# Performance work log

Hardware: AMD Instinct MI355X
Metric: run time of the kernel (lower is better)

The kernel has to match this reference:

```python
import jax, jax.numpy as jnp
import numpy as np

B, T, Rn, D, O, E, H, C, TM = 20, 20, 20, 4096, 16, 512, 8, 68, 1900


def l2norm(x, axis=-1, eps=1e-12):
    return x / jnp.maximum(jnp.linalg.norm(x, axis=axis, keepdims=True), eps)


def setup_inputs() -> dict:
    key = jax.random.key(0)
    ks = jax.random.split(key, 10)
    return {
        "features": jax.random.normal(ks[0], (B, T, Rn, D), jnp.float32),
        "labels": jax.random.randint(ks[1], (B, O), 0, C),
        "temporal_mem": jax.random.normal(ks[2], (TM, T, D), jnp.float32),
        "entity_W": jax.random.normal(ks[3], (C, E), jnp.float32) / np.float32(np.sqrt(C)),
        "entity_b": jnp.zeros((E,), jnp.float32),
        "Wq": jax.random.normal(ks[4], (E, E), jnp.float32) / np.float32(np.sqrt(E)),
        "Wk": jax.random.normal(ks[5], (D, E), jnp.float32) / np.float32(np.sqrt(D)),
        "Wv": jax.random.normal(ks[6], (D, E), jnp.float32) / np.float32(np.sqrt(D)),
        "Wo": jax.random.normal(ks[7], (E, E), jnp.float32) / np.float32(np.sqrt(E)),
        "obj_W1": jax.random.normal(ks[8], (D, E), jnp.float32) / np.float32(np.sqrt(D)),
        "obj_b1": jnp.zeros((E,), jnp.float32),
        "obj_W2": jax.random.normal(ks[9], (E, 1), jnp.float32) / np.float32(np.sqrt(E)),
        "obj_b2": jnp.zeros((1,), jnp.float32),
    }


def reference(features, labels, temporal_mem, entity_W, entity_b, Wq, Wk, Wv, Wo,
              obj_W1, obj_b1, obj_W2, obj_b2):
    beta = 0.5   # loss mixing weight (module's beta)
    qgce = 0.7   # generalized-CE exponent
    Dh = E // H
    # region features, L2-normalized (dataset_feat == 'CVPR' path)
    Rf = l2norm(features)                                   # [B,T,Rn,D]

    # ---- temporal memory-bank kNN retrieval ----
    R_max = l2norm(jnp.max(Rf, axis=2))                     # [B,T,D] max-pool over regions
    mem_max = l2norm(jnp.max(temporal_mem, axis=1))         # [TM,D] max-pool over frames
    sim = jnp.einsum('btd,md->btm', R_max, mem_max)         # [B,T,TM]
    idx = jnp.argmax(sim, axis=-1)                          # [B,T] nearest memory slot
    Rp = temporal_mem[idx]                                  # [B,T,T,D] gathered memory videos
    mem_feat = jnp.max(Rp, axis=2)                          # [B,T,D]

    # ---- entity (object-label) embedding: one-hot with class 0 zeroed ----
    onehot = jax.nn.one_hot(labels, C, dtype=features.dtype)
    onehot = onehot * (labels != 0)[..., None].astype(features.dtype)
    Qe = onehot @ entity_W + entity_b                       # [B,O,E]

    # ---- multi-head attention fusion over regions + retrieved memory ----
    kv = jnp.concatenate([Rf.reshape(B, T * Rn, D), mem_feat], axis=1)  # [B,N,D]
    q = (Qe @ Wq).reshape(B, O, H, Dh)
    k = (kv @ Wk).reshape(B, -1, H, Dh)
    v = (kv @ Wv).reshape(B, -1, H, Dh)
    scores = jnp.einsum('bohd,bnhd->bhon', q, k) / np.float32(np.sqrt(Dh))
    attn = jax.nn.softmax(scores, axis=-1)
    fused = jnp.einsum('bhon,bnhd->bohd', attn, v).reshape(B, O, E) @ Wo  # [B,O,E]

    # ---- top-k region objectness selection + generalized CE ----
    QR = jax.lax.stop_gradient(jnp.mean(scores, axis=1)[:, :, :T * Rn].reshape(B, O, T, Rn))
    hi = jnp.argmax(QR, axis=-1)                            # [B,O,T] top-1 region
    lo = jnp.argmin(QR, axis=-1)                            # [B,O,T] low region
    bidx = jnp.arange(B)[:, None, None]
    tidx = jnp.arange(T)[None, None, :]
    R_high = Rf[bidx, tidx, hi]                             # [B,O,T,D]
    R_low = Rf[bidx, tidx, lo]                              # [B,O,T,D]
    osel = (labels != 0).astype(features.dtype)             # [B,O]
    onum = jnp.maximum(jnp.sum(osel, axis=1), 1.0)
    mlp = lambda x: jax.nn.sigmoid(jnp.tanh(x @ obj_W1 + obj_b1) @ obj_W2 + obj_b2)
    s_hi = mlp(R_high * osel[..., None, None]).squeeze(-1)  # [B,O,T]
    s_lo = mlp(R_low * osel[..., None, None]).squeeze(-1)
    gce_hi = jnp.mean((1.0 - (s_hi + 1e-7) ** qgce) / qgce * osel[..., None], axis=-1)
    gce_lo = jnp.mean((1.0 - (1.0 - s_lo + 1e-7) ** qgce) / qgce * osel[..., None], axis=-1)
    gce = jnp.mean(jnp.sum(gce_hi, axis=1) / onum) + jnp.mean(jnp.sum(gce_lo, axis=1) / onum)

    return fused + beta * gce
```

## Files before the change

kernel.cpp:

```cpp
#include <hip/hip_runtime.h>

#define B_   20
#define T_   20
#define RN   20
#define D_   4096
#define O_   16
#define E_   512
#define H_   8
#define DH   64
#define TM_  1900
#define NKV  420
#define MROWS (B_*NKV)
#define MPAD 8448
#define NW   1536
#define NSIM 1920
#define MSIM 512
#define CAP  256
#define SIMK 8

using f32x4  = __attribute__((ext_vector_type(4))) float;
using bf16x8 = __attribute__((ext_vector_type(8))) __bf16;

__device__ __forceinline__ unsigned short f2bf(float f){
  unsigned u = __float_as_uint(f);
  u += 0x7fffu + ((u >> 16) & 1u);
  return (unsigned short)(u >> 16);
}

__device__ __forceinline__ void st_bf4(unsigned short* dst, float4 v){
  ushort4 o = make_ushort4(f2bf(v.x), f2bf(v.y), f2bf(v.z), f2bf(v.w));
  *(ushort4*)dst = o;
}

__device__ __forceinline__ float bsum256(float v, float* sh){
  int t = threadIdx.x;
  for (int o = 32; o; o >>= 1) v += __shfl_down(v, o, 64);
  __syncthreads();
  if ((t & 63) == 0) sh[t >> 6] = v;
  __syncthreads();
  return sh[0] + sh[1] + sh[2] + sh[3];
}

__device__ __forceinline__ float bmax256(float v, float* sh){
  int t = threadIdx.x;
  for (int o = 32; o; o >>= 1) v = fmaxf(v, __shfl_down(v, o, 64));
  __syncthreads();
  if ((t & 63) == 0) sh[t >> 6] = v;
  __syncthreads();
  return fmaxf(fmaxf(sh[0], sh[1]), fmaxf(sh[2], sh[3]));
}

__device__ __forceinline__ void gld16(const void* g, void* l){
  __builtin_amdgcn_global_load_lds(
      (const __attribute__((address_space(1))) unsigned int*)g,
      (__attribute__((address_space(3))) unsigned int*)l, 16, 0, 0);
}

__global__ __launch_bounds__(256) void k_pre(
    const float* __restrict__ F, const float* __restrict__ TMm,
    const float* __restrict__ Wk, const float* __restrict__ Wv, const float* __restrict__ W1,
    unsigned short* __restrict__ Wall,
    unsigned short* __restrict__ A, float* __restrict__ rmaxr, float* __restrict__ rmsum,
    unsigned short* __restrict__ ubf,
    float* __restrict__ umax, float* __restrict__ msum, unsigned short* __restrict__ wnorm,
    const int* __restrict__ labels, const float* __restrict__ entW, const float* __restrict__ entB,
    const float* __restrict__ Wq, float* __restrict__ q){
  __shared__ char smem[4352];
  int bid = blockIdx.x, t = threadIdx.x;
  if (bid < 1920){
    int m = bid;
    if (m >= TM_){
      int4 zz = make_int4(0,0,0,0);
      int4* row = (int4*)(wnorm + (size_t)m*D_);
      row[t] = zz; row[t + 256] = zz;
      return;
    }
    float* sh = (float*)smem;
    const float* base = TMm + (size_t)m*T_*D_;
    float4 mx[4];
#pragma unroll
    for (int i = 0; i < 4; ++i) mx[i] = make_float4(-1e30f,-1e30f,-1e30f,-1e30f);
    for (int f = 0; f < T_; ++f){
#pragma unroll
      for (int i = 0; i < 4; ++i){
        float4 v = *(const float4*)(base + (size_t)f*D_ + i*1024 + t*4);
        mx[i].x = fmaxf(mx[i].x, v.x); mx[i].y = fmaxf(mx[i].y, v.y);
        mx[i].z = fmaxf(mx[i].z, v.z); mx[i].w = fmaxf(mx[i].w, v.w);
      }
    }
    float s = 0.f;
#pragma unroll
    for (int i = 0; i < 4; ++i){
      *(float4*)(umax + (size_t)m*D_ + i*1024 + t*4) = mx[i];
      s += mx[i].x*mx[i].x + mx[i].y*mx[i].y + mx[i].z*mx[i].z + mx[i].w*mx[i].w;
    }
    s = bsum256(s, sh);
    if (t == 0) msum[m] = s;
    float inv = 1.f / fmaxf(sqrtf(s), 1e-12f);
#pragma unroll
    for (int i = 0; i < 4; ++i){
      float4 u = mx[i];
      u.x *= inv; u.y *= inv; u.z *= inv; u.w *= inv;
      st_bf4(wnorm + (size_t)m*D_ + i*1024 + t*4, u);
    }
  } else if (bid < 2432){
    int bt = bid - 1920;
    if (bt >= 400){
      int4 zz = make_int4(0,0,0,0);
      int4* row = (int4*)(ubf + (size_t)bt*D_);
      row[t] = zz; row[t + 256] = zz;
      return;
    }
    float* sh = (float*)smem;
    int b = bt / T_, tt = bt % T_;
    const float* fb = F + (size_t)bt*RN*D_;
    unsigned short* ab = A + ((size_t)b*NKV + (size_t)tt*RN)*D_;
    float4 mx[4];
#pragma unroll
    for (int i = 0; i < 4; ++i) mx[i] = make_float4(-1e30f,-1e30f,-1e30f,-1e30f);
    for (int r = 0; r < RN; ++r){
      float4 v[4];
      float s = 0.f;
#pragma unroll
      for (int i = 0; i < 4; ++i){
        v[i] = *(const float4*)(fb + (size_t)r*D_ + i*1024 + t*4);
        s += v[i].x*v[i].x + v[i].y*v[i].y + v[i].z*v[i].z + v[i].w*v[i].w;
      }
      s = bsum256(s, sh);
      float ri = 1.f / fmaxf(sqrtf(s), 1e-12f);
#pragma unroll
      for (int i = 0; i < 4; ++i){
        v[i].x *= ri; v[i].y *= ri; v[i].z *= ri; v[i].w *= ri;
        st_bf4(ab + (size_t)r*D_ + i*1024 + t*4, v[i]);
        mx[i].x = fmaxf(mx[i].x, v[i].x); mx[i].y = fmaxf(mx[i].y, v[i].y);
        mx[i].z = fmaxf(mx[i].z, v[i].z); mx[i].w = fmaxf(mx[i].w, v[i].w);
      }
    }
    float s2 = 0.f;
#pragma unroll
    for (int i = 0; i < 4; ++i){
      *(float4*)(rmaxr + (size_t)bt*D_ + i*1024 + t*4) = mx[i];
      s2 += mx[i].x*mx[i].x + mx[i].y*mx[i].y + mx[i].z*mx[i].z + mx[i].w*mx[i].w;
    }
    s2 = bsum256(s2, sh);
    if (t == 0) rmsum[bt] = s2;
    float inv = 1.f / fmaxf(sqrtf(s2), 1e-12f);
#pragma unroll
    for (int i = 0; i < 4; ++i){
      float4 u = mx[i];
      u.x *= inv; u.y *= inv; u.z *= inv; u.w *= inv;
      st_bf4(ubf + (size_t)bt*D_ + i*1024 + t*4, u);
    }
  } else if (bid < 8576){
    int wti = bid - 2432;
    float* tile = (float*)smem;
    int kb = (wti & 127) * 32, nb = (wti >> 7) * 32;
    const float* src; int nc0;
    if (nb < 512)      { src = Wk; nc0 = nb; }
    else if (nb < 1024){ src = Wv; nc0 = nb - 512; }
    else               { src = W1; nc0 = nb - 1024; }
    int tx = t & 31, ty = t >> 5;
#pragma unroll
    for (int j = 0; j < 4; ++j){
      int k = kb + ty + j*8;
      tile[(ty + j*8)*33 + tx] = src[(size_t)k*E_ + nc0 + tx];
    }
    __syncthreads();
#pragma unroll
    for (int j = 0; j < 4; ++j){
      int n = nb + ty + j*8;
      int k = kb + tx;
      Wall[(size_t)n*D_ + k] = f2bf(tile[tx*33 + ty + j*8]);
    }
  } else {
    int bo = bid - 8576;
    float* qe = (float*)smem;
    int lab = labels[bo];
    float sel = (lab != 0) ? 1.f : 0.f;
    qe[t]       = sel * entW[(size_t)lab*E_ + t]       + entB[t];
    qe[t + 256] = sel * entW[(size_t)lab*E_ + t + 256] + entB[t + 256];
    __syncthreads();
    float a0 = 0.f, a1 = 0.f;
    for (int ep = 0; ep < E_; ++ep){
      float r = qe[ep];
      a0 += r * Wq[(size_t)ep*E_ + t];
      a1 += r * Wq[(size_t)ep*E_ + t + 256];
    }
    q[(size_t)bo*E_ + t] = a0;
    q[(size_t)bo*E_ + t + 256] = a1;
  }
}

__global__ __launch_bounds__(256, 2) void k_gemm(const unsigned short* __restrict__ A,
                                                 const unsigned short* __restrict__ Bw,
                                                 float* __restrict__ C,
                                                 int nNt, int ldc, int doswz, int nwg,
                                                 int nblk, int nkt, size_t cpart){
  __shared__ char lds[32768];
  int part = blockIdx.x / nblk;
  int bid  = blockIdx.x % nblk;
  if (doswz){ int q = nwg >> 3; bid = (bid & 7)*q + (bid >> 3); }
  int mt = bid / nNt, nt = bid % nNt;
  int tid = threadIdx.x, wv = tid >> 6, l = tid & 63;
  int wr = (wv >> 1) * 64, wc = (wv & 1) * 64;
  const char* Ab = (const char*)A + (size_t)mt*128*(size_t)(D_*2);
  const char* Bb = (const char*)Bw + (size_t)nt*128*(size_t)(D_*2);
  C += (size_t)part * cpart;
  f32x4 acc[4][4];
#pragma unroll
  for (int m = 0; m < 4; ++m)
#pragma unroll
    for (int n = 0; n < 4; ++n) acc[m][n] = (f32x4){0.f,0.f,0.f,0.f};
  int kt0 = part * nkt;
  for (int kt = kt0; kt < kt0 + nkt; ++kt){
    int ktoff = kt*128;
#pragma unroll
    for (int i = 0; i < 4; ++i){
      int idx = i*256 + tid;
      int row = idx >> 3, u = idx & 7;
      int ul = u ^ (row & 7);
      gld16(Ab + (size_t)row*(D_*2) + ktoff + ul*16, lds + i*4096 + wv*1024);
      gld16(Bb + (size_t)row*(D_*2) + ktoff + ul*16, lds + 16384 + i*4096 + wv*1024);
    }
    __syncthreads();
#pragma unroll
    for (int kk = 0; kk < 2; ++kk){
      bf16x8 av[4], bv[4];
#pragma unroll
      for (int m = 0; m < 4; ++m){
        int row = wr + m*16 + (l & 15);
        int u = (kk*4 + (l >> 4)) ^ (row & 7);
        av[m] = *(const bf16x8*)(lds + row*128 + u*16);
      }
#pragma unroll
      for (int n = 0; n < 4; ++n){
        int row = wc + n*16 + (l & 15);
        int u = (kk*4 + (l >> 4)) ^ (row & 7);
        bv[n] = *(const bf16x8*)(lds + 16384 + row*128 + u*16);
      }
#pragma unroll
      for (int m = 0; m < 4; ++m)
#pragma unroll
        for (int n = 0; n < 4; ++n)
          acc[m][n] = __builtin_amdgcn_mfma_f32_16x16x32_bf16(av[m], bv[n], acc[m][n], 0, 0, 0);
    }
    __syncthreads();
  }
  int rq = (l >> 4) * 4, cq = l & 15;
  size_t crow0 = (size_t)mt*128 + wr, ccol0 = (size_t)nt*128 + wc;
#pragma unroll
  for (int m = 0; m < 4; ++m)
#pragma unroll
    for (int n = 0; n < 4; ++n){
      size_t r0 = crow0 + m*16 + rq, c0 = ccol0 + n*16 + cq;
#pragma unroll
      for (int j = 0; j < 4; ++j)
        C[(r0 + j)*ldc + c0] = acc[m][n][j];
    }
}

__global__ __launch_bounds__(256) void k_pick(const float* __restrict__ simp,
                                              const float* __restrict__ rmaxr, const float* __restrict__ rmsum,
                                              const float* __restrict__ umax, const float* __restrict__ msum,
                                              unsigned short* __restrict__ A){
  int bt = blockIdx.x, t = threadIdx.x;
  if (bt >= 400){
    int4 z = make_int4(0,0,0,0);
    int4* row = (int4*)(A + (size_t)(MROWS + bt - 400)*D_);
    row[t] = z; row[t + 256] = z;
    return;
  }
  __shared__ float srow[NSIM];
  __shared__ float sh[4];
  __shared__ int cnt;
  __shared__ int cl[CAP];
  for (int m = t; m < NSIM; m += 256){
    float s = 0.f;
#pragma unroll
    for (int p = 0; p < SIMK; ++p)
      s += simp[(size_t)p*MSIM*NSIM + (size_t)bt*NSIM + m];
    srow[m] = s;
  }
  if (t == 0) cnt = 0;
  __syncthreads();
  float mx = -1e30f;
  for (int m = t; m < TM_; m += 256) mx = fmaxf(mx, srow[m]);
  mx = bmax256(mx, sh);
  float thr = mx - 2.5e-4f;
  for (int m = t; m < TM_; m += 256){
    if (srow[m] >= thr){
      int p = atomicAdd(&cnt, 1);
      if (p < CAP) cl[p] = m;
    }
  }
  __syncthreads();
  int cn = cnt < CAP ? cnt : CAP;
  float rinvv = 1.f / fmaxf(sqrtf(rmsum[bt]), 1e-12f);
  const float* a = rmaxr + (size_t)bt*D_;
  float best = -1e30f; int bestm = 0x7fffffff;
  for (int ci = 0; ci < cn; ++ci){
    int m = cl[ci];
    const float* wrow = umax + (size_t)m*D_;
    float p = 0.f;
    for (int i = t*4; i < D_; i += 1024){
      float4 av = *(const float4*)(a + i);
      float4 wv = *(const float4*)(wrow + i);
      p += av.x*wv.x + av.y*wv.y + av.z*wv.z + av.w*wv.w;
    }
    p = bsum256(p, sh);
    float sim = p * rinvv * (1.f / fmaxf(sqrtf(msum[m]), 1e-12f));
    if (sim > best || (sim == best && m < bestm)){ best = sim; bestm = m; }
  }
  int b = bt / T_, tt = bt % T_;
  unsigned short* dst = A + ((size_t)b*NKV + 400 + tt)*D_;
  const float* src = umax + (size_t)bestm*D_;
#pragma unroll
  for (int i = 0; i < 4; ++i){
    size_t off = (size_t)i*1024 + t*4;
    float4 v = *(const float4*)(src + off);
    st_bf4(dst + off, v);
  }
}

__global__ __launch_bounds__(256) void k_post(const float* __restrict__ q, const float* __restrict__ c2,
                                              float* __restrict__ fpre, int* __restrict__ hi,
                                              int* __restrict__ lo, const float* __restrict__ b1,
                                              const float* __restrict__ W2, const float* __restrict__ b2,
                                              float* __restrict__ z){
  __shared__ char smem[58368];
  int bid = blockIdx.x, t = threadIdx.x;
  if (bid < 160){
    int b = bid >> 3, h = bid & 7;
    int w = t >> 6, l = t & 63;
    float* qhp = (float*)smem;
    float* kb  = (float*)(smem + 4160);
    float* sc  = (float*)(smem + 31460);
    for (int i = t; i < O_*DH; i += 256){
      int o = i >> 6, d = i & 63;
      qhp[o*65 + d] = q[((size_t)(b*O_ + o))*E_ + h*DH + d] * 0.125f;
    }
    __syncthreads();
    for (int c = 0; c < 4; ++c){
      for (int i = t; i < 105*DH; i += 256){
        int j = i >> 6, d = i & 63;
        kb[j*65 + d] = c2[((size_t)(b*NKV + c*105 + j))*NW + h*DH + d];
      }
      __syncthreads();
      for (int i = t; i < O_*105; i += 256){
        int o = i / 105, j = i % 105;
        float acc = 0.f;
        for (int d = 0; d < DH; ++d) acc += qhp[o*65 + d] * kb[j*65 + d];
        sc[o*420 + c*105 + j] = acc;
      }
      __syncthreads();
    }
    for (int oi = 0; oi < 4; ++oi){
      int o = w + oi*4;
      float mx = -1e30f;
      for (int n = l; n < NKV; n += 64) mx = fmaxf(mx, sc[o*420 + n]);
      for (int of = 32; of; of >>= 1) mx = fmaxf(mx, __shfl_xor(mx, of, 64));
      float sum = 0.f;
      for (int n = l; n < NKV; n += 64){ float e = expf(sc[o*420 + n] - mx); sc[o*420 + n] = e; sum += e; }
      for (int of = 32; of; of >>= 1) sum += __shfl_xor(sum, of, 64);
      float inv = 1.f / sum;
      for (int n = l; n < NKV; n += 64) sc[o*420 + n] *= inv;
    }
    __syncthreads();
    float acc[4] = {0.f, 0.f, 0.f, 0.f};
    for (int c = 0; c < 4; ++c){
      for (int i = t; i < 105*DH; i += 256){
        int j = i >> 6, d = i & 63;
        kb[j*65 + d] = c2[((size_t)(b*NKV + c*105 + j))*NW + E_ + h*DH + d];
      }
      __syncthreads();
#pragma unroll
      for (int og = 0; og < 4; ++og){
        int o = og*4 + w;
        float a = 0.f;
        for (int j = 0; j < 105; ++j) a += sc[o*420 + c*105 + j] * kb[j*65 + l];
        acc[og] += a;
      }
      __syncthreads();
    }
#pragma unroll
    for (int og = 0; og < 4; ++og){
      int o = og*4 + w;
      fpre[((size_t)(b*O_ + o))*E_ + h*DH + l] = acc[og];
    }
  } else if (bid < 560){
    int bt = bid - 160;
    int b = bt / T_, tt = bt % T_;
    float* kl = (float*)smem;
    float* qr = (float*)(smem + 41040);
    for (int i = t; i < RN*E_; i += 256){
      int r = i >> 9, e = i & 511;
      kl[r*513 + e] = c2[((size_t)(b*NKV + tt*RN + r))*NW + e];
    }
    __syncthreads();
#pragma unroll
    for (int pp = 0; pp < 2; ++pp){
      int p = t + pp*256;
      if (p < O_*RN){
        int o = p / RN, r = p % RN;
        const float* qrow = q + ((size_t)(b*O_ + o))*E_;
        float acc = 0.f;
        for (int e = 0; e < E_; ++e) acc += qrow[e] * kl[r*513 + e];
        qr[o*20 + r] = acc;
      }
    }
    __syncthreads();
    if (t < O_){
      int o = t;
      float bh = qr[o*20], bl = qr[o*20]; int ih = 0, il = 0;
#pragma unroll
      for (int r = 1; r < RN; ++r){
        float v = qr[o*20 + r];
        if (v > bh){ bh = v; ih = r; }
        if (v < bl){ bl = v; il = r; }
      }
      int rowbase = b*NKV + tt*RN;
      int outi = (b*O_ + o)*T_ + tt;
      hi[outi] = rowbase + ih;
      lo[outi] = rowbase + il;
    }
  } else {
    int g = (bid - 560)*4 + (t >> 6);
    int l = t & 63;
    int b = g / 400, j = g % 400;
    int row = b*NKV + j;
    const float* hrow = c2 + (size_t)row*NW + 1024;
    float acc = 0.f;
    for (int e = l; e < E_; e += 64) acc += tanhf(hrow[e] + b1[e]) * W2[e];
    for (int of = 32; of; of >>= 1) acc += __shfl_down(acc, of, 64);
    if (l == 0) z[row] = 1.f / (1.f + expf(-(acc + b2[0])));
  }
}

__global__ __launch_bounds__(256) void k_outg(const float* __restrict__ fpre, const float* __restrict__ Wo,
                                              const float* __restrict__ z, const int* __restrict__ hi,
                                              const int* __restrict__ lo, const int* __restrict__ labels,
                                              float* __restrict__ out){
  int bo = blockIdx.x, t = threadIdx.x;
  __shared__ float rowv[E_];
  __shared__ float vb[B_];
  __shared__ int cb[B_];
  __shared__ float gsh;
  rowv[t] = fpre[(size_t)bo*E_ + t];
  rowv[t + 256] = fpre[(size_t)bo*E_ + t + 256];
  if (t < B_){ vb[t] = 0.f; cb[t] = 0; }
  __syncthreads();
  for (int p = t; p < B_*O_; p += 256){
    int b = p / O_;
    if (labels[p] != 0){
      float acc = 0.f;
      for (int tt = 0; tt < T_; ++tt){
        float shi = z[hi[p*T_ + tt]];
        float slo = z[lo[p*T_ + tt]];
        acc += (1.f - __powf(shi + 1e-7f, 0.7f)) / 0.7f;
        acc += (1.f - __powf(1.f - slo + 1e-7f, 0.7f)) / 0.7f;
      }
      atomicAdd(&vb[b], acc / (float)T_);
      atomicAdd(&cb[b], 1);
    }
  }
  __syncthreads();
  if (t == 0){
    float g = 0.f;
    for (int b = 0; b < B_; ++b) g += vb[b] / fmaxf((float)cb[b], 1.f);
    gsh = 0.5f * (g / (float)B_);
  }
  __syncthreads();
  float g = gsh;
  float a0 = 0.f, a1 = 0.f;
  for (int ep = 0; ep < E_; ++ep){
    float r = rowv[ep];
    a0 += r * Wo[(size_t)ep*E_ + t];
    a1 += r * Wo[(size_t)ep*E_ + t + 256];
  }
  out[(size_t)bo*E_ + t] = a0 + g;
  out[(size_t)bo*E_ + t + 256] = a1 + g;
}

extern "C" void kernel_launch(void* const* d_in, const int* in_sizes, int n_in,
                              void* d_out, int out_size, void* d_ws, size_t ws_size,
                              hipStream_t stream) {
  (void)in_sizes; (void)n_in; (void)out_size; (void)ws_size;
  const float* F    = (const float*)d_in[0];
  const int*   labels = (const int*)d_in[1];
  const float* TMm  = (const float*)d_in[2];
  const float* entW = (const float*)d_in[3];
  const float* entB = (const float*)d_in[4];
  const float* Wq   = (const float*)d_in[5];
  const float* Wk   = (const float*)d_in[6];
  const float* Wv   = (const float*)d_in[7];
  const float* Wo   = (const float*)d_in[8];
  const float* W1   = (const float*)d_in[9];
  const float* b1   = (const float*)d_in[10];
  const float* W2   = (const float*)d_in[11];
  const float* b2   = (const float*)d_in[12];
  float* out = (float*)d_out;

  size_t off = 0;
  char* wsb = (char*)d_ws;
  auto alloc = [&](size_t bytes) -> char* {
    char* p = wsb + off; off += (bytes + 255) & ~(size_t)255; return p;
  };
  unsigned short* A_kv = (unsigned short*)alloc((size_t)MPAD * D_ * 2);
  unsigned short* Wall = (unsigned short*)alloc((size_t)NW * D_ * 2);
  float* umax          = (float*)alloc((size_t)TM_ * D_ * 4);
  char*  c2reg         = alloc((size_t)MPAD * NW * 4);
  float* C2    = (float*)c2reg;
  unsigned short* wnorm = (unsigned short*)c2reg;
  float* simp  = (float*)(c2reg + 15728640);
  unsigned short* ubf = (unsigned short*)alloc((size_t)MSIM * D_ * 2);
  float* rmaxr = (float*)alloc((size_t)400 * D_ * 4);
  float* qbuf  = (float*)alloc((size_t)B_ * O_ * E_ * 4);
  float* fpre  = (float*)alloc((size_t)B_ * O_ * E_ * 4);
  float* rmsum = (float*)alloc(400 * 4);
  float* msum  = (float*)alloc(TM_ * 4);
  int*   hib   = (int*)alloc(6400 * 4);
  int*   lob   = (int*)alloc(6400 * 4);
  float* zbuf  = (float*)alloc((size_t)MROWS * 4);

  k_pre<<<8896, 256, 0, stream>>>(F, TMm, Wk, Wv, W1, Wall, A_kv, rmaxr, rmsum, ubf,
                                  umax, msum, wnorm, labels, entW, entB, Wq, qbuf);
  k_gemm<<<(MSIM/128)*(NSIM/128)*SIMK, 256, 0, stream>>>(ubf, wnorm, simp, NSIM/128, NSIM, 0, 60,
                                                         (MSIM/128)*(NSIM/128), (D_/64)/SIMK,
                                                         (size_t)MSIM*NSIM);
  k_pick<<<448, 256, 0, stream>>>(simp, rmaxr, rmsum, umax, msum, A_kv);
  k_gemm<<<(MPAD/128)*(NW/128), 256, 0, stream>>>(A_kv, Wall, C2, NW/128, NW, 1,
                                                  (MPAD/128)*(NW/128),
                                                  (MPAD/128)*(NW/128), D_/64, 0);
  k_post<<<2560, 256, 0, stream>>>(qbuf, C2, fpre, hib, lob, b1, W2, b2, zbuf);
  k_outg<<<B_*O_, 256, 0, stream>>>(fpre, Wo, zbuf, hib, lob, labels, out);
}
```

Baseline: 510.7 us.

## Use 256x256 tiled double-buffered GEMM kernel for main KV/objectness projection

Replaces the 128x128-tile GEMM used for the large A_kv x Wall projection with a new 256x256-tile kernel using 512 threads, 128KB LDS double buffering, XCD-aware block remapping and raised wave priority around MFMA sections. Larger tiles raise arithmetic intensity and halve global reloads of A and B. The launch shrinks to 33x6=198 workgroups at one block per CU, so wave count and occupancy drop and the grid may underfill the machine's CUs.

```diff
diff --git a/kernel.cpp b/kernel.cpp
--- a/kernel.cpp
+++ b/kernel.cpp
@@ -253,6 +253,102 @@
 #pragma unroll
     for (int n = 0; n < 4; ++n){
       size_t r0 = crow0 + m*16 + rq, c0 = ccol0 + n*16 + cq;
+#pragma unroll
+      for (int j = 0; j < 4; ++j)
+        C[(r0 + j)*ldc + c0] = acc[m][n][j];
+    }
+}
+
+__global__ __launch_bounds__(512, 1) void k_gemm256(const unsigned short* __restrict__ A,
+                                                    const unsigned short* __restrict__ Bw,
+                                                    float* __restrict__ C,
+                                                    int nNt, int ldc, int nwg){
+  __shared__ char lds[131072];
+  int bid = blockIdx.x;
+  {
+    int q8 = nwg >> 3, r8 = nwg & 7, x = bid & 7, s = bid >> 3;
+    bid = (x < r8 ? x*(q8+1) : r8*(q8+1) + (x-r8)*q8) + s;
+  }
+  int mt = bid / nNt, nt = bid % nNt;
+  int tid = threadIdx.x, wid = tid >> 6, l = tid & 63;
+  int wr = (wid >> 2) * 128;
+  int wc = (wid & 3) * 64;
+  int fr = l & 15, fq = l >> 4;
+  const char* Ab = (const char*)A + (size_t)mt*256*(size_t)(D_*2);
+  const char* Bb = (const char*)Bw + (size_t)nt*256*(size_t)(D_*2);
+  f32x4 acc[8][4];
+#pragma unroll
+  for (int m = 0; m < 8; ++m)
+#pragma unroll
+    for (int n = 0; n < 4; ++n) acc[m][n] = (f32x4){0.f,0.f,0.f,0.f};
+
+#pragma unroll
+  for (int i = 0; i < 4; ++i){
+    int idx = i*512 + tid;
+    int row = idx >> 3, u = idx & 7;
+    int ul = u ^ (row & 7);
+    gld16(Ab + (size_t)row*(D_*2) + (size_t)(ul*16), lds + idx*16);
+    gld16(Bb + (size_t)row*(D_*2) + (size_t)(ul*16), lds + 32768 + idx*16);
+  }
+  __syncthreads();
+
+  int c = 0;
+  for (int kt = 0; kt < D_/64; ++kt){
+    if (kt < D_/64 - 1){
+      int ktoff = (kt + 1) * 128;
+      char* dA = lds + (c^1)*65536;
+      char* dB = dA + 32768;
+#pragma unroll
+      for (int i = 0; i < 4; ++i){
+        int idx = i*512 + tid;
+        int row = idx >> 3, u = idx & 7;
+        int ul = u ^ (row & 7);
+        gld16(Ab + (size_t)row*(D_*2) + ktoff + ul*16, dA + idx*16);
+        gld16(Bb + (size_t)row*(D_*2) + ktoff + ul*16, dB + idx*16);
+      }
+    }
+    const char* LA = lds + c*65536;
+    const char* LB = LA + 32768;
+    bf16x8 bv[4][2];
+#pragma unroll
+    for (int n = 0; n < 4; ++n)
+#pragma unroll
+      for (int kk = 0; kk < 2; ++kk){
+        int row = wc + n*16 + fr;
+        int u = (kk*4 + fq) ^ (row & 7);
+        bv[n][kk] = *(const bf16x8*)(LB + row*128 + u*16);
+      }
+    __builtin_amdgcn_s_setprio(1);
+#pragma unroll
+    for (int mp = 0; mp < 4; ++mp){
+      bf16x8 av[2][2];
+#pragma unroll
+      for (int mm = 0; mm < 2; ++mm)
+#pragma unroll
+        for (int kk = 0; kk < 2; ++kk){
+          int row = wr + (mp*2 + mm)*16 + fr;
+          int u = (kk*4 + fq) ^ (row & 7);
+          av[mm][kk] = *(const bf16x8*)(LA + row*128 + u*16);
+        }
+#pragma unroll
+      for (int mm = 0; mm < 2; ++mm)
+#pragma unroll
+        for (int n = 0; n < 4; ++n)
+#pragma unroll
+          for (int kk = 0; kk < 2; ++kk)
+            acc[mp*2 + mm][n] = __builtin_amdgcn_mfma_f32_16x16x32_bf16(
+                av[mm][kk], bv[n][kk], acc[mp*2 + mm][n], 0, 0, 0);
+    }
+    __builtin_amdgcn_s_setprio(0);
+    __syncthreads();
+    c ^= 1;
+  }
+  size_t crow0 = (size_t)mt*256 + wr, ccol0 = (size_t)nt*256 + wc;
+#pragma unroll
+  for (int m = 0; m < 8; ++m)
+#pragma unroll
+    for (int n = 0; n < 4; ++n){
+      size_t r0 = crow0 + m*16 + fq*4, c0 = ccol0 + n*16 + fr;
 #pragma unroll
       for (int j = 0; j < 4; ++j)
         C[(r0 + j)*ldc + c0] = acc[m][n][j];
@@ -528,9 +624,8 @@
                                                          (MSIM/128)*(NSIM/128), (D_/64)/SIMK,
                                                          (size_t)MSIM*NSIM);
   k_pick<<<448, 256, 0, stream>>>(simp, rmaxr, rmsum, umax, msum, A_kv);
-  k_gemm<<<(MPAD/128)*(NW/128), 256, 0, stream>>>(A_kv, Wall, C2, NW/128, NW, 1,
-                                                  (MPAD/128)*(NW/128),
-                                                  (MPAD/128)*(NW/128), D_/64, 0);
+  k_gemm256<<<(MPAD/256)*(NW/256), 512, 0, stream>>>(A_kv, Wall, C2, NW/256, NW,
+                                                     (MPAD/256)*(NW/256));
   k_post<<<2560, 256, 0, stream>>>(qbuf, C2, fpre, hib, lob, b1, W2, b2, zbuf);
   k_outg<<<B_*O_, 256, 0, stream>>>(fpre, Wo, zbuf, hib, lob, labels, out);
 }
```

Result: no change. 501.9 us (-1.7%).
